# Performance work log

Measured on AMD Instinct MI355X. Metric: run time of the kernel, lower is better.

## Reference

```python
import jax, jax.numpy as jnp
import numpy as np

BS, L, D, N = 4, 2048, 1024, 16

def setup_inputs() -> dict:
    key = jax.random.key(0)
    ks = jax.random.split(key, 8)
    s = 1.0 / np.sqrt(D)
    x  = jax.random.normal(ks[0], (BS, L, D), dtype=jnp.float32)
    # torch Linear params; stored transposed so y = x @ W + b
    W1 = jax.random.uniform(ks[1], (D, D), jnp.float32, -s, s)
    b1 = jax.random.uniform(ks[2], (D,),   jnp.float32, -s, s)
    W2 = jax.random.uniform(ks[3], (D, N), jnp.float32, -s, s)
    b2 = jax.random.uniform(ks[4], (N,),   jnp.float32, -s, s)
    W3 = jax.random.uniform(ks[5], (D, N), jnp.float32, -s, s)
    b3 = jax.random.uniform(ks[6], (N,),   jnp.float32, -s, s)
    A  = jax.random.normal(ks[7], (D, N),  jnp.float32) * np.sqrt(2.0 / (D + N))  # xavier
    return {"x": x, "W1": W1, "b1": b1, "W2": W2, "b2": b2, "W3": W3, "b3": b3, "A": A}

def reference(x, W1, b1, W2, b2, W3, b3, A):
    # S6 forward (non-recurrent branch).
    B = x @ W2 + b2                     # (b,l,n)
    C = x @ W3 + b3                     # (b,l,n)
    delta = jax.nn.softplus(x @ W1 + b1)  # (b,l,d)
    # dA = exp(einsum('bld,dn->bldn', delta, A)) is multiplied by an all-zero h
    # in the original forward, so it does not affect the output (dead code under DCE).
    dB = jnp.einsum('bld,bln->bldn', delta, B)   # (b,l,d,n) -- 512 MB intermediate
    h = x[..., None] * dB                         # (b,l,d,n)
    y = jnp.einsum('bln,bldn->bld', C, h)         # (b,l,d)
    return y
```

## Files before the change

### kernel.cpp

```cpp
#include <hip/hip_runtime.h>
#include <hip/hip_bf16.h>
#include <math.h>


namespace {

constexpr int Dd   = 1024;
constexpr int ROWS = 8192;

typedef __bf16 bf16x8 __attribute__((ext_vector_type(8)));
typedef float  floatx4 __attribute__((ext_vector_type(4)));

#define LDS_BAR() asm volatile("s_waitcnt lgkmcnt(0)\n\ts_barrier" ::: "memory")

__device__ __forceinline__ float softplus_fast(float v) {
    float l = __logf(1.0f + __expf(v));
    return v > 15.0f ? v : l;
}
__device__ __forceinline__ float bf_lo(unsigned short u) {
    union { unsigned q; float f; } c; c.q = ((unsigned)u) << 16; return c.f;
}

__global__ __launch_bounds__(256) void w23_kernel(
    const float* __restrict__ W2, const float* __restrict__ W3,
    __bf16* __restrict__ W2t, __bf16* __restrict__ W3t)
{
    const int t  = threadIdx.x;
    const int n  = t >> 4;
    const int k0 = blockIdx.x * 64 + (t & 15) * 4;
    ushort4 a, b;
    union { __bf16 h; unsigned short u; } c;
    c.h = (__bf16)W2[(size_t)(k0 + 0) * 16 + n]; a.x = c.u;
    c.h = (__bf16)W2[(size_t)(k0 + 1) * 16 + n]; a.y = c.u;
    c.h = (__bf16)W2[(size_t)(k0 + 2) * 16 + n]; a.z = c.u;
    c.h = (__bf16)W2[(size_t)(k0 + 3) * 16 + n]; a.w = c.u;
    c.h = (__bf16)W3[(size_t)(k0 + 0) * 16 + n]; b.x = c.u;
    c.h = (__bf16)W3[(size_t)(k0 + 1) * 16 + n]; b.y = c.u;
    c.h = (__bf16)W3[(size_t)(k0 + 2) * 16 + n]; b.z = c.u;
    c.h = (__bf16)W3[(size_t)(k0 + 3) * 16 + n]; b.w = c.u;
    *(ushort4*)&W2t[(size_t)n * Dd + k0] = a;
    *(ushort4*)&W3t[(size_t)n * Dd + k0] = b;
}

__global__ __launch_bounds__(256, 4) void prep_kernel(
    const float* __restrict__ X, const float* __restrict__ W1,
    const __bf16* __restrict__ W2t, const float* __restrict__ b2,
    const __bf16* __restrict__ W3t, const float* __restrict__ b3,
    __bf16* __restrict__ Xb, __bf16* __restrict__ W1t, float* __restrict__ Sv)
{
    const int t = threadIdx.x;

    if (blockIdx.x >= 512) {
        __shared__ __bf16 tile[64][66];
        const int bidx = blockIdx.x - 512;
        const int bi = bidx >> 4, bj = bidx & 15;
        const int c = t & 63, r4 = t >> 6;
        #pragma unroll
        for (int i = 0; i < 16; ++i) {
            const int r = i * 4 + r4;
            tile[r][c] = (__bf16)W1[(size_t)(bi * 64 + r) * Dd + bj * 64 + c];
        }
        __syncthreads();
        #pragma unroll
        for (int i = 0; i < 16; ++i) {
            const int r = i * 4 + r4;
            W1t[(size_t)(bj * 64 + r) * Dd + bi * 64 + c] = tile[c][r];
        }
        return;
    }

    __shared__ float red[4][2][16][16];
    const int w = t >> 6, lane = t & 63;
    const int l15 = lane & 15, quad = lane >> 4;
    const int row0 = blockIdx.x * 16;
    const int kw = w * 256;
    const size_t xoff = (size_t)(row0 + l15) * Dd;
    const size_t woff = (size_t)l15 * Dd;

    floatx4 acc0 = {0.f, 0.f, 0.f, 0.f}, acc1 = {0.f, 0.f, 0.f, 0.f};
    #pragma unroll
    for (int ks = 0; ks < 8; ++ks) {
        const int k0 = kw + ks * 32 + quad * 8;
        const float4 xa = *(const float4*)&X[xoff + k0];
        const float4 xb = *(const float4*)&X[xoff + k0 + 4];
        bf16x8 af;
        af[0] = (__bf16)xa.x; af[1] = (__bf16)xa.y;
        af[2] = (__bf16)xa.z; af[3] = (__bf16)xa.w;
        af[4] = (__bf16)xb.x; af[5] = (__bf16)xb.y;
        af[6] = (__bf16)xb.z; af[7] = (__bf16)xb.w;
        *(bf16x8*)&Xb[xoff + k0] = af;
        const bf16x8 w2f = *(const bf16x8*)&W2t[woff + k0];
        const bf16x8 w3f = *(const bf16x8*)&W3t[woff + k0];
        acc0 = __builtin_amdgcn_mfma_f32_16x16x32_bf16(af, w2f, acc0, 0, 0, 0);
        acc1 = __builtin_amdgcn_mfma_f32_16x16x32_bf16(af, w3f, acc1, 0, 0, 0);
    }
    #pragma unroll
    for (int r = 0; r < 4; ++r) {
        red[w][0][quad * 4 + r][l15] = acc0[r];
        red[w][1][quad * 4 + r][l15] = acc1[r];
    }
    __syncthreads();
    {
        const int r = t >> 4, n = t & 15;
        float B = b2[n], C = b3[n];
        #pragma unroll
        for (int ww = 0; ww < 4; ++ww) {
            B += red[ww][0][r][n];
            C += red[ww][1][r][n];
        }
        float p = B * C;
        p += __shfl_xor(p, 1); p += __shfl_xor(p, 2);
        p += __shfl_xor(p, 4); p += __shfl_xor(p, 8);
        if (n == 0) Sv[row0 + r] = p;
    }
}

__global__ __launch_bounds__(256, 2) void gemm_kernel(
    const __bf16* __restrict__ Xb, const __bf16* __restrict__ W1t,
    const float* __restrict__ Sv, const float* __restrict__ b1,
    float* __restrict__ Y)
{
    __shared__ __attribute__((aligned(16))) __bf16 lds[8192];
    const int t = threadIdx.x, lane = t & 63;
    const int w = t >> 6, wm = w & 1, wn = w >> 1;
    const int l15 = lane & 15, quad = lane >> 4;
    const int cb = blockIdx.x & 7, rb = blockIdx.x >> 3;
    const int row0 = rb * 128, col0 = cb * 128;

    floatx4 acc[4][4] = {};

    const __bf16* gA[2]; const __bf16* gB[2];
    int dA[2], dB[2];
    #pragma unroll
    for (int r = 0; r < 2; ++r) {
        const int u = r * 256 + t;
        const int p = u >> 3, s = u & 7, c4 = s ^ (p & 7);
        const int rowL = 2 * p + (c4 >> 2), chk = c4 & 3;
        gA[r] = Xb  + (size_t)(row0 + rowL) * Dd + chk * 8;
        gB[r] = W1t + (size_t)(col0 + rowL) * Dd + chk * 8;
        dA[r] = u * 8;
        dB[r] = 4096 + u * 8;
    }

    bf16x8 bufA[2][2], bufB[2][2];

    auto gload = [&](int buf, int k) {
        #pragma unroll
        for (int r = 0; r < 2; ++r) {
            bufA[buf][r] = *(const bf16x8*)(gA[r] + k);
            bufB[buf][r] = *(const bf16x8*)(gB[r] + k);
        }
    };
    auto store_lds = [&](int buf) {
        #pragma unroll
        for (int r = 0; r < 2; ++r) {
            *(bf16x8*)&lds[dA[r]] = bufA[buf][r];
            *(bf16x8*)&lds[dB[r]] = bufB[buf][r];
        }
    };
    auto compute = [&]() {
        bf16x8 af[4], bfr[4];
        #pragma unroll
        for (int mt = 0; mt < 4; ++mt) {
            const int rl = wm * 64 + mt * 16 + l15;
            const int p = rl >> 1, c4 = ((rl & 1) << 2) | quad, s = c4 ^ (p & 7);
            af[mt] = *(const bf16x8*)&lds[p * 64 + s * 8];
        }
        #pragma unroll
        for (int nt = 0; nt < 4; ++nt) {
            const int nl = wn * 64 + nt * 16 + l15;
            const int p = nl >> 1, c4 = ((nl & 1) << 2) | quad, s = c4 ^ (p & 7);
            bfr[nt] = *(const bf16x8*)&lds[4096 + p * 64 + s * 8];
        }
        #pragma unroll
        for (int mt = 0; mt < 4; ++mt)
            #pragma unroll
            for (int nt = 0; nt < 4; ++nt)
                acc[mt][nt] = __builtin_amdgcn_mfma_f32_16x16x32_bf16(
                    af[mt], bfr[nt], acc[mt][nt], 0, 0, 0);
    };

    gload(0, 0);
    for (int k0 = 0; k0 < Dd; k0 += 64) {
        gload(1, k0 + 32);
        LDS_BAR();
        store_lds(0);
        LDS_BAR();
        compute();
        if (k0 + 64 < Dd) gload(0, k0 + 64);
        LDS_BAR();
        store_lds(1);
        LDS_BAR();
        compute();
    }

    float bias[4];
    #pragma unroll
    for (int nt = 0; nt < 4; ++nt) bias[nt] = b1[col0 + wn * 64 + nt * 16 + l15];

    #pragma unroll
    for (int mt = 0; mt < 4; ++mt) {
        #pragma unroll
        for (int rr = 0; rr < 4; ++rr) {
            const int row = row0 + wm * 64 + mt * 16 + quad * 4 + rr;
            const float sv = Sv[row];
            const unsigned short* xrow =
                (const unsigned short*)(Xb + (size_t)row * Dd + col0);
            float* yrow = Y + (size_t)row * Dd + col0;
            #pragma unroll
            for (int nt = 0; nt < 4; ++nt) {
                const int cl = wn * 64 + nt * 16 + l15;
                const float v  = acc[mt][nt][rr] + bias[nt];
                const float sp = softplus_fast(v);
                yrow[cl] = bf_lo(xrow[cl]) * sp * sv;
            }
        }
    }
}

}

extern "C" void kernel_launch(void* const* d_in, const int* in_sizes, int n_in,
                              void* d_out, int out_size, void* d_ws, size_t ws_size,
                              hipStream_t stream)
{
    const float* X  = (const float*)d_in[0];
    const float* W1 = (const float*)d_in[1];
    const float* b1 = (const float*)d_in[2];
    const float* W2 = (const float*)d_in[3];
    const float* b2 = (const float*)d_in[4];
    const float* W3 = (const float*)d_in[5];
    const float* b3 = (const float*)d_in[6];
    float* Y = (float*)d_out;

    char* ws = (char*)d_ws;
    __bf16* Xb  = (__bf16*)ws;
    __bf16* W1t = (__bf16*)(ws + 16777216);
    float*  Sv  = (float*) (ws + 16777216 + 2097152);
    __bf16* W2t = (__bf16*)(ws + 16777216 + 2097152 + 32768);
    __bf16* W3t = (__bf16*)(ws + 16777216 + 2097152 + 65536);

    hipLaunchKernelGGL(w23_kernel, dim3(16), dim3(256), 0, stream, W2, W3, W2t, W3t);
    hipLaunchKernelGGL(prep_kernel, dim3(768), dim3(256), 0, stream,
                       X, W1, W2t, b2, W3t, b3, Xb, W1t, Sv);
    hipLaunchKernelGGL(gemm_kernel, dim3((ROWS / 128) * (Dd / 128)), dim3(256), 0, stream,
                       Xb, W1t, Sv, b1, Y);
}
```

Measured before the change: 135.4 us.

## Use direct global-to-LDS loads with triple-buffered pipeline in GEMM

The GEMM main loop now uses global_load_lds to copy tiles straight from global memory into LDS. This replaces the register-staged load plus LDS store. LDS becomes a three-stage ring buffer, so tiles two steps ahead are in flight while the current one is computed, and each step needs one barrier with a vmcnt wait instead of four barriers. This raises LDS use from 16 KB to 48 KB per block, which may reduce occupancy, and correctness depends on the manual vmcnt counting and the LDS layout that global_load_lds writes.

```diff
diff --git a/kernel.cpp b/kernel.cpp
--- a/kernel.cpp
+++ b/kernel.cpp
@@ -3,6 +3,9 @@
 #include <math.h>
 
 
+#define GLB(p) ((const __attribute__((address_space(1))) void*)(p))
+#define LDSP(p) ((__attribute__((address_space(3))) void*)(p))
+
 namespace {
 
 constexpr int Dd   = 1024;
@@ -10,8 +13,6 @@
 
 typedef __bf16 bf16x8 __attribute__((ext_vector_type(8)));
 typedef float  floatx4 __attribute__((ext_vector_type(4)));
-
-#define LDS_BAR() asm volatile("s_waitcnt lgkmcnt(0)\n\ts_barrier" ::: "memory")
 
 __device__ __forceinline__ float softplus_fast(float v) {
     float l = __logf(1.0f + __expf(v));
@@ -120,7 +121,7 @@
     const float* __restrict__ Sv, const float* __restrict__ b1,
     float* __restrict__ Y)
 {
-    __shared__ __attribute__((aligned(16))) __bf16 lds[8192];
+    __shared__ __attribute__((aligned(16))) __bf16 lds[3 * 8192];
     const int t = threadIdx.x, lane = t & 63;
     const int w = t >> 6, wm = w & 1, wn = w >> 1;
     const int l15 = lane & 15, quad = lane >> 4;
@@ -142,35 +143,30 @@
         dB[r] = 4096 + u * 8;
     }
 
-    bf16x8 bufA[2][2], bufB[2][2];
-
-    auto gload = [&](int buf, int k) {
+    auto issue = [&](int tt, int c) {
+        const int base = c * 8192;
         #pragma unroll
         for (int r = 0; r < 2; ++r) {
-            bufA[buf][r] = *(const bf16x8*)(gA[r] + k);
-            bufB[buf][r] = *(const bf16x8*)(gB[r] + k);
+            __builtin_amdgcn_global_load_lds(GLB(gA[r] + tt * 32),
+                                             LDSP(&lds[base + dA[r]]), 16, 0, 0);
+            __builtin_amdgcn_global_load_lds(GLB(gB[r] + tt * 32),
+                                             LDSP(&lds[base + dB[r]]), 16, 0, 0);
         }
     };
-    auto store_lds = [&](int buf) {
-        #pragma unroll
-        for (int r = 0; r < 2; ++r) {
-            *(bf16x8*)&lds[dA[r]] = bufA[buf][r];
-            *(bf16x8*)&lds[dB[r]] = bufB[buf][r];
-        }
-    };
-    auto compute = [&]() {
+    auto compute = [&](int c) {
+        const int base = c * 8192;
         bf16x8 af[4], bfr[4];
         #pragma unroll
         for (int mt = 0; mt < 4; ++mt) {
             const int rl = wm * 64 + mt * 16 + l15;
             const int p = rl >> 1, c4 = ((rl & 1) << 2) | quad, s = c4 ^ (p & 7);
-            af[mt] = *(const bf16x8*)&lds[p * 64 + s * 8];
+            af[mt] = *(const bf16x8*)&lds[base + p * 64 + s * 8];
         }
         #pragma unroll
         for (int nt = 0; nt < 4; ++nt) {
             const int nl = wn * 64 + nt * 16 + l15;
             const int p = nl >> 1, c4 = ((nl & 1) << 2) | quad, s = c4 ^ (p & 7);
-            bfr[nt] = *(const bf16x8*)&lds[4096 + p * 64 + s * 8];
+            bfr[nt] = *(const bf16x8*)&lds[base + 4096 + p * 64 + s * 8];
         }
         #pragma unroll
         for (int mt = 0; mt < 4; ++mt)
@@ -180,18 +176,17 @@
                     af[mt], bfr[nt], acc[mt][nt], 0, 0, 0);
     };
 
-    gload(0, 0);
-    for (int k0 = 0; k0 < Dd; k0 += 64) {
-        gload(1, k0 + 32);
-        LDS_BAR();
-        store_lds(0);
-        LDS_BAR();
-        compute();
-        if (k0 + 64 < Dd) gload(0, k0 + 64);
-        LDS_BAR();
-        store_lds(1);
-        LDS_BAR();
-        compute();
+    issue(0, 0);
+    issue(1, 1);
+    #pragma unroll
+    for (int tt = 0; tt < 32; ++tt) {
+        if (tt == 31) {
+            asm volatile("s_waitcnt vmcnt(0) lgkmcnt(0)\n\ts_barrier" ::: "memory");
+        } else {
+            asm volatile("s_waitcnt vmcnt(4) lgkmcnt(0)\n\ts_barrier" ::: "memory");
+        }
+        if (tt + 2 < 32) issue(tt + 2, (tt + 2) % 3);
+        compute(tt % 3);
     }
 
     float bias[4];
```

Result: slower. 147.2 us (+8.7%).
